# Optimization experiments

Hardware: AMD Instinct MI355X
Metric: run time of the kernel (lower is better)

The kernel has to match this reference:

```python
import jax, jax.numpy as jnp
import numpy as np
from jax.scipy.linalg import solve_triangular

B = 131072; OBS = 128; AD = 8; H = 64; FH = 32; NL = 4
D1 = AD // 2; D2 = AD - D1; TRIL = AD * (AD + 1) // 2
_rows, _cols = np.tril_indices(AD)          # same row-major order as torch.tril_indices
_diag = (_rows == _cols)                    # bool mask over TRIL entries
_diag_pos = np.where(_diag)[0]
LOG2PI = float(np.log(2.0 * np.pi))
EPS = float(np.finfo(np.float32).eps)       # torch RMSNorm default eps = finfo.eps


def _rms(x, w):
    return x * jax.lax.rsqrt(jnp.mean(x * x, axis=-1, keepdims=True) + EPS) * w


def setup_inputs() -> dict:
    ks = iter(jax.random.split(jax.random.key(0), 32))
    def w(shape, scale):
        return jax.random.normal(next(ks), shape, jnp.float32) * scale
    z = lambda *s: jnp.zeros(s, jnp.float32)
    return dict(
        x=jax.random.normal(next(ks), (B, OBS), jnp.float32),
        action=jax.random.normal(next(ks), (B, AD), jnp.float32),
        z_rpo=jax.random.uniform(next(ks), (B, AD), jnp.float32, -0.1, 0.1),
        cW1=w((OBS, H), OBS ** -0.5), cb1=z(H), c_rms=jnp.ones(H, jnp.float32),
        cW2=w((H, H), H ** -0.5), cb2=z(H), cW3=w((H, 1), H ** -0.5), cb3=z(1),
        aW1=w((OBS, H), OBS ** -0.5), ab1=z(H), aW2=w((H, H), H ** -0.5), ab2=z(H),
        mW=w((H, AD), 0.01), mb=z(AD),
        tW1=w((OBS, H), OBS ** -0.5), tb1=z(H), t_rms1=jnp.ones(H, jnp.float32),
        tW2=w((H, H), H ** -0.5), tb2=z(H), t_rms2=jnp.ones(H, jnp.float32),
        hW=w((H, TRIL), 0.01), hb=z(TRIL),
        fW1=w((NL, D1 + OBS, FH), (D1 + OBS) ** -0.5), fb1=z(NL, FH),
        fW2=w((NL, FH, 2 * D2), 0.01), fb2=z(NL, 2 * D2),
    )


def reference(x, action, z_rpo, cW1, cb1, c_rms, cW2, cb2, cW3, cb3,
              aW1, ab1, aW2, ab2, mW, mb,
              tW1, tb1, t_rms1, tW2, tb2, t_rms2, hW, hb,
              fW1, fb1, fW2, fb2):
    silu = jax.nn.silu
    Bn = x.shape[0]
    # actor mean trunk + head, with RPO uniform perturbation (action is given)
    h = silu(silu(x @ aW1 + ab1) @ aW2 + ab2)
    action_mean = h @ mW + mb + z_rpo
    # state-dependent lower-triangular covariance factor
    tl = _rms(silu(x @ tW1 + tb1), t_rms1)
    tl = _rms(silu(tl @ tW2 + tb2), t_rms2)
    raw = tl @ hW + hb                                   # [B, TRIL]
    proc = jnp.where(_diag, jax.nn.softplus(raw), raw)
    L = jnp.zeros((Bn, AD, AD), raw.dtype).at[:, _rows, _cols].set(proc)
    log_det_L = jnp.log(proc[:, _diag_pos]).sum(-1)      # [B]
    # coupling flow inverse: noise -> correlated
    noise = action - action_mean
    x1, x2 = noise[:, :D1], noise[:, D1:]
    fld = jnp.zeros((Bn,), raw.dtype)
    for i in reversed(range(NL)):
        cond, y = (x1, x2) if i % 2 == 0 else (x2, x1)
        st = silu(jnp.concatenate([cond, x], -1) @ fW1[i] + fb1[i]) @ fW2[i] + fb2[i]
        s_raw, tshift = jnp.split(st, 2, -1)
        s = jnp.tanh(s_raw) * 2.0
        xt = (y - tshift) * jnp.exp(-s)
        if i % 2 == 0:
            x2 = xt
        else:
            x1 = xt
        fld = fld + s.sum(-1)
    correlated = jnp.concatenate([x1, x2], -1)           # [B, AD]
    zc = solve_triangular(L, correlated[..., None], lower=True)[..., 0]
    mahal = (zc * zc).sum(-1)
    log_prob = -0.5 * (AD * LOG2PI + mahal) - log_det_L - fld
    entropy = 0.5 * (AD * (1.0 + LOG2PI)) + log_det_L + fld
    # critic
    v = _rms(silu(x @ cW1 + cb1), c_rms)
    v = silu(v @ cW2 + cb2) @ cW3 + cb3                  # [B, 1]
    return (action, log_prob, entropy, v)
```

## Files before the change

kernel.cpp:

```cpp
#include <hip/hip_runtime.h>
#include <hip/hip_bf16.h>

typedef __attribute__((ext_vector_type(8))) short    v8s;
typedef __attribute__((ext_vector_type(4))) float    f4;
typedef __attribute__((ext_vector_type(2))) float    f2;
typedef __attribute__((ext_vector_type(2))) unsigned u32x2;

#define MFMA16 __builtin_amdgcn_mfma_f32_16x16x32_bf16

#define AW1T 0
#define TW1T 8192
#define CW1T 16384
#define AW2T 24576
#define TW2T 28672
#define CW2T 32768
#define MWT  36864
#define HWT  37888
#define FW1XT 40960
#define FW2T  57344
#define WS_BF16_TOTAL 59392
#define W1CTO 0
#define HBPO  512

#define LOG2PI 1.83787706640934548356f
#define EPSF   1.1920928955078125e-07f

__device__ __constant__ int PERM[36] = {0,2,5,9,14,20,27,35,
  1,3,4,6,7,8,10,11,12,13,15,16,17,18,19,21,22,23,24,25,26,28,29,30,31,32,33,34};

__device__ __forceinline__ float ubits(unsigned u){union{unsigned u;float f;}c;c.u=u;return c.f;}
__device__ __forceinline__ unsigned fbits(float f){union{float f;unsigned u;}c;c.f=f;return c.u;}
__device__ __forceinline__ float rcpf(float x){ return __builtin_amdgcn_rcpf(x); }
__device__ __forceinline__ float siluf(float v){ return v * rcpf(1.f + __expf(-v)); }
__device__ __forceinline__ unsigned pk2(float a,float b){
  union{__hip_bfloat162 h; unsigned u;} cv;
  cv.h = __float22bfloat162_rn(make_float2(a,b));
  return cv.u;
}
__device__ __forceinline__ unsigned short f2bu(float a){
  unsigned ua=fbits(a); ua+=0x7fffu+((ua>>16)&1u);
  return (unsigned short)(ua>>16);
}
__device__ __forceinline__ float b2f16(unsigned short h){ return ubits(((unsigned)h)<<16); }
__device__ __forceinline__ float qsum(float v){
  v += __shfl_xor(v,16,64); v += __shfl_xor(v,32,64); return v;
}
__device__ __forceinline__ int swz(int row, int blk){ return row*64 + ((blk ^ (row&7))*8); }
__device__ __forceinline__ int swzx(int row, int blk){ return row*128 + ((blk ^ (row&7))*8); }
__device__ __forceinline__ int a2idx(int i, int n, int c){
  return ((((i<<5)+n)<<4) ^ ((n&8)<<1)) + (c ^ ((n&7)<<1));
}

__global__ __launch_bounds__(256)
void prep_kernel(const float* __restrict__ aW1, const float* __restrict__ aW2,
                 const float* __restrict__ mW,  const float* __restrict__ tW1,
                 const float* __restrict__ tW2, const float* __restrict__ hW,
                 const float* __restrict__ hb,  const float* __restrict__ cW1,
                 const float* __restrict__ cW2, const float* __restrict__ fW1,
                 const float* __restrict__ fW2,
                 unsigned short* __restrict__ ws16, float* __restrict__ wsf)
{
  const int tid = blockIdx.x*256 + threadIdx.x;
  const int stride = gridDim.x*256;
  for (int idx=tid; idx<64*128; idx+=stride){
    int f=idx>>9, r=idx&511, lane=r>>3, j=idx&7;
    int wt=f>>2, kt=f&3, c=lane&15, q=lane>>4;
    int n=wt*16+c, k=kt*32+q*8+j;
    ws16[AW1T+idx]=f2bu(aW1[k*64+n]);
    ws16[TW1T+idx]=f2bu(tW1[k*64+n]);
    ws16[CW1T+idx]=f2bu(cW1[k*64+n]);
  }
  for (int idx=tid; idx<64*64; idx+=stride){
    int f=idx>>9, r=idx&511, lane=r>>3, j=idx&7;
    int wt=f>>1, kt=f&1, c=lane&15, q=lane>>4;
    int n=wt*16+c, k=kt*32+q*8+j;
    ws16[AW2T+idx]=f2bu(aW2[k*64+n]);
    ws16[TW2T+idx]=f2bu(tW2[k*64+n]);
    ws16[CW2T+idx]=f2bu(cW2[k*64+n]);
  }
  for (int idx=tid; idx<16*64; idx+=stride){
    int f=idx>>9, r=idx&511, lane=r>>3, j=idx&7;
    int kt=f, c=lane&15, q=lane>>4;
    int n=c, k=kt*32+q*8+j;
    ws16[MWT+idx]=f2bu(n<8 ? mW[k*8+n] : 0.f);
  }
  for (int idx=tid; idx<48*64; idx+=stride){
    int f=idx>>9, r=idx&511, lane=r>>3, j=idx&7;
    int wt=f>>1, kt=f&1, c=lane&15, q=lane>>4;
    int n=wt*16+c, k=kt*32+q*8+j;
    ws16[HWT+idx]=f2bu(n<36 ? hW[k*36+PERM[n]] : 0.f);
  }
  for (int idx=tid; idx<4*32*128; idx+=stride){
    int i=idx>>12, rem=idx&4095;
    int f=rem>>9, r=rem&511, lane=r>>3, j=idx&7;
    int wt=f>>2, kt=f&3, c=lane&15, q=lane>>4;
    int n=wt*16+c, k=kt*32+q*8+j;
    ws16[FW1XT+idx]=f2bu(fW1[i*4224 + (4+k)*32 + n]);
  }
  for (int idx=tid; idx<4*16*32; idx+=stride){
    int i=idx>>9, r=idx&511, lane=r>>3, j=idx&7;
    int c=lane&15, q=lane>>4;
    int k=q*8+j;
    ws16[FW2T+idx]=f2bu(c<8 ? fW2[i*256 + k*8 + c] : 0.f);
  }
  for (int idx=tid; idx<4*32*4; idx+=stride){
    int i=idx>>7, rem=idx&127, n=rem>>2, k=rem&3;
    wsf[W1CTO+idx]=fW1[i*4224 + k*32 + n];
  }
  for (int idx=tid; idx<48; idx+=stride)
    wsf[HBPO+idx] = idx<36 ? hb[PERM[idx]] : 0.f;
}

template<int NWT>
__device__ __forceinline__ void gemmX(const unsigned short* __restrict__ Wt,
                                      const v8s* __restrict__ xf,
                                      f4 (*acc)[2], int lane)
{
#pragma unroll
  for (int kt=0; kt<4; ++kt){
    v8s wf[NWT];
#pragma unroll
    for (int wt=0; wt<NWT; ++wt)
      wf[wt] = *(const v8s*)(Wt + ((wt*4 + kt)*64 + lane)*8);
#pragma unroll
    for (int wt=0; wt<NWT; ++wt)
#pragma unroll
      for (int et=0; et<2; ++et)
        acc[wt][et] = MFMA16(wf[wt], xf[et*4+kt], acc[wt][et], 0,0,0);
  }
}

template<int NWT>
__device__ __forceinline__ void gemmH(const unsigned short* __restrict__ Wt,
                                      const unsigned short* __restrict__ actL,
                                      f4 (*acc)[2], int lane, int c, int q)
{
#pragma unroll
  for (int kt=0; kt<2; ++kt){
    v8s wf[NWT];
#pragma unroll
    for (int wt=0; wt<NWT; ++wt)
      wf[wt] = *(const v8s*)(Wt + ((wt*2 + kt)*64 + lane)*8);
    v8s af[2];
#pragma unroll
    for (int et=0; et<2; ++et)
      af[et] = *(const v8s*)(actL + swz(et*16+c, kt*4+q));
#pragma unroll
    for (int wt=0; wt<NWT; ++wt)
#pragma unroll
      for (int et=0; et<2; ++et)
        acc[wt][et] = MFMA16(wf[wt], af[et], acc[wt][et], 0,0,0);
  }
}

__global__ __launch_bounds__(128) __attribute__((amdgpu_waves_per_eu(3, 4)))
void policy_kernel(
    const float* __restrict__ x,    const float* __restrict__ action, const float* __restrict__ z_rpo,
    const float* __restrict__ cb1,  const float* __restrict__ c_rms,  const float* __restrict__ cb2,
    const float* __restrict__ cW3,  const float* __restrict__ cb3,
    const float* __restrict__ ab1,  const float* __restrict__ ab2,    const float* __restrict__ mb,
    const float* __restrict__ tb1,  const float* __restrict__ t_rms1, const float* __restrict__ tb2,
    const float* __restrict__ t_rms2,
    const float* __restrict__ fb1,  const float* __restrict__ fb2,
    const unsigned short* __restrict__ ws16, const float* __restrict__ wsf,
    float* __restrict__ out, const int Btot)
{
  const int tid  = threadIdx.x;
  const int wv   = tid >> 6;
  const int lane = tid & 63;
  const int q = lane >> 4, c = lane & 15;
  const int b0 = blockIdx.x << 5;

  __shared__ alignas(16) unsigned char smem[20352];
  unsigned*       a2b  = (unsigned*)smem;
  unsigned short* xL   = (unsigned short*)smem;
  unsigned short* act0 = (unsigned short*)(smem + 8192);
  unsigned short* act1 = (unsigned short*)(smem + 12288);
  unsigned short* triL = (unsigned short*)(smem + 16384);
  float*          nstL = (float*)(smem + 18688);
  unsigned short* amL  = (unsigned short*)(smem + 19712);
  float*          fldL = (float*)(smem + 20224);

  {
    const float* xb = x + (size_t)b0*128;
    const int rr = lane>>3, bb = (lane&7)*2;
#pragma unroll
    for (int rg=0; rg<2; ++rg){
      const int row = wv*16 + rg*8 + rr;
      const float* p = xb + row*128 + (lane&7)*16;
      f4 u0=*(const f4*)p, u1=*(const f4*)(p+4), u2=*(const f4*)(p+8), u3=*(const f4*)(p+12);
      union { unsigned u[4]; v8s v; } r0, r1;
      r0.u[0]=pk2(u0[0],u0[1]); r0.u[1]=pk2(u0[2],u0[3]);
      r0.u[2]=pk2(u1[0],u1[1]); r0.u[3]=pk2(u1[2],u1[3]);
      r1.u[0]=pk2(u2[0],u2[1]); r1.u[1]=pk2(u2[2],u2[3]);
      r1.u[2]=pk2(u3[0],u3[1]); r1.u[3]=pk2(u3[2],u3[3]);
      *(v8s*)(xL + swzx(row, bb  )) = r0.v;
      *(v8s*)(xL + swzx(row, bb+1)) = r1.v;
    }
  }
  const int l = lane;
  f4 a0v, a1v, zr0v, zr1v;
  if (wv==0 && l<32){
    const size_t bb = (size_t)(b0+l)*8;
    a0v=*(const f4*)(action+bb); a1v=*(const f4*)(action+bb+4);
    zr0v=*(const f4*)(z_rpo+bb); zr1v=*(const f4*)(z_rpo+bb+4);
    *(f4*)(out+bb)=a0v; *(f4*)(out+bb+4)=a1v;
  }
  __syncthreads();
  v8s xf[8];
#pragma unroll
  for (int et=0; et<2; ++et)
#pragma unroll
    for (int kt=0; kt<4; ++kt)
      xf[et*4+kt] = *(const v8s*)(xL + swzx(et*16+c, kt*4+q));
  __syncthreads();

  f4 acc[4][2];
  const f4 z4 = {0.f,0.f,0.f,0.f};
  float ldet[2], vv[2];
  float tri[36];

  if (wv == 0){
#pragma unroll
    for (int wt=0; wt<4; ++wt) for (int et=0; et<2; ++et) acc[wt][et]=z4;
    gemmX<4>(ws16+AW1T, xf, acc, lane);
#pragma unroll
    for (int wt=0; wt<4; ++wt){
      const f4 bv = *(const f4*)(ab1 + wt*16 + q*4);
#pragma unroll
      for (int et=0; et<2; ++et){
        float s0=siluf(acc[wt][et][0]+bv[0]), s1=siluf(acc[wt][et][1]+bv[1]);
        float s2=siluf(acc[wt][et][2]+bv[2]), s3=siluf(acc[wt][et][3]+bv[3]);
        u32x2 u = {pk2(s0,s1), pk2(s2,s3)};
        *(u32x2*)(act0 + swz(et*16+c, wt*2+(q>>1)) + (q&1)*4) = u;
      }
    }
#pragma unroll
    for (int wt=0; wt<4; ++wt) for (int et=0; et<2; ++et) acc[wt][et]=z4;
    gemmH<4>(ws16+AW2T, act0, acc, lane, c, q);
#pragma unroll
    for (int wt=0; wt<4; ++wt){
      const f4 bv = *(const f4*)(ab2 + wt*16 + q*4);
#pragma unroll
      for (int et=0; et<2; ++et){
        float s0=siluf(acc[wt][et][0]+bv[0]), s1=siluf(acc[wt][et][1]+bv[1]);
        float s2=siluf(acc[wt][et][2]+bv[2]), s3=siluf(acc[wt][et][3]+bv[3]);
        u32x2 u = {pk2(s0,s1), pk2(s2,s3)};
        *(u32x2*)(act0 + swz(et*16+c, wt*2+(q>>1)) + (q&1)*4) = u;
      }
    }
    {
      f4 am1[1][2]; am1[0][0]=z4; am1[0][1]=z4;
      gemmH<1>(ws16+MWT, act0, am1, lane, c, q);
      if (q<2){
        const f4 mbv = *(const f4*)(mb + q*4);
#pragma unroll
        for (int et=0; et<2; ++et){
          u32x2 u = {pk2(am1[0][et][0]+mbv[0], am1[0][et][1]+mbv[1]),
                     pk2(am1[0][et][2]+mbv[2], am1[0][et][3]+mbv[3])};
          *(u32x2*)(amL + (et*16+c)*8 + q*4) = u;
        }
      }
    }
  } else {
#pragma unroll
    for (int i=0; i<4; ++i){
      f4 a2[2][2];
#pragma unroll
      for (int wt=0; wt<2; ++wt) for (int et=0; et<2; ++et) a2[wt][et]=z4;
      gemmX<2>(ws16+FW1XT+i*4096, xf, a2, lane);
#pragma unroll
      for (int wt=0; wt<2; ++wt)
#pragma unroll
        for (int r=0; r<4; ++r){
          const int n = wt*16 + q*4 + r;
          a2b[a2idx(i, n, c)] = pk2(a2[wt][0][r], a2[wt][1][r]);
        }
    }
  }

  if (wv==0 && l<32){
    float nst[8];
#pragma unroll
    for (int j=0;j<4;++j){
      nst[j]   = a0v[j]-b2f16(amL[l*8+j])  -zr0v[j];
      nst[4+j] = a1v[j]-b2f16(amL[l*8+4+j])-zr1v[j];
    }
    *(f4*)(nstL + l*8)     = (f4){nst[0],nst[1],nst[2],nst[3]};
    *(f4*)(nstL + l*8 + 4) = (f4){nst[4],nst[5],nst[6],nst[7]};
  }

  __syncthreads();

  if (wv == 0){
    float fld = 0.f;
    const int e = l & 31, h = l >> 5, j0 = h*2;
#pragma unroll
    for (int ii=0; ii<4; ++ii){
      const int i = 3-ii;
      const int cb = (i&1)?4:0, yb = (i&1)?0:4;
      float nv[2][4];
#pragma unroll
      for (int et=0; et<2; ++et){
        const float* np = nstL + (et*16+c)*8 + cb;
        f2 t0=*(const f2*)np, t1=*(const f2*)(np+2);
        nv[et][0]=t0[0]; nv[et][1]=t0[1]; nv[et][2]=t1[0]; nv[et][3]=t1[1];
      }
#pragma unroll
      for (int wt=0; wt<2; ++wt){
        const f4 bv = *(const f4*)(fb1 + i*32 + wt*16 + q*4);
        float sh[2][4];
#pragma unroll
        for (int r=0; r<4; ++r){
          const int n = wt*16 + q*4 + r;
          const f4 wc = *(const f4*)(wsf + W1CTO + i*128 + n*4);
          const unsigned ua = a2b[a2idx(i, n, c)];
          const float a2e0 = b2f16((unsigned short)(ua & 0xffffu));
          const float a2e1 = b2f16((unsigned short)(ua >> 16));
          {
            float hv0 = a2e0 + bv[r]
                      + wc[0]*nv[0][0] + wc[1]*nv[0][1]
                      + wc[2]*nv[0][2] + wc[3]*nv[0][3];
            sh[0][r] = siluf(hv0);
            float hv1 = a2e1 + bv[r]
                      + wc[0]*nv[1][0] + wc[1]*nv[1][1]
                      + wc[2]*nv[1][2] + wc[3]*nv[1][3];
            sh[1][r] = siluf(hv1);
          }
        }
#pragma unroll
        for (int et=0; et<2; ++et){
          u32x2 u = {pk2(sh[et][0],sh[et][1]), pk2(sh[et][2],sh[et][3])};
          *(u32x2*)(act0 + swz(et*16+c, wt*2+(q>>1)) + (q&1)*4) = u;
        }
      }
      {
        const v8s wf3 = *(const v8s*)(ws16 + FW2T + i*512 + lane*8);
        f4 as[2];
#pragma unroll
        for (int et=0; et<2; ++et){
          const v8s hf = *(const v8s*)(act0 + swz(et*16+c, q));
          f4 a1s = z4;
          a1s = MFMA16(wf3, hf, a1s, 0,0,0);
          as[et]=a1s;
        }
        if (q<2){
          const f4 fbv = *(const f4*)(fb2 + i*8 + q*4);
#pragma unroll
          for (int et=0; et<2; ++et){
            u32x2 u = {pk2(as[et][0]+fbv[0], as[et][1]+fbv[1]),
                       pk2(as[et][2]+fbv[2], as[et][3]+fbv[3])};
            *(u32x2*)(amL + (et*16+c)*8 + q*4) = u;
          }
        }
      }
      {
        float sr0=b2f16(amL[e*8+j0  ]), sr1=b2f16(amL[e*8+j0+1]);
        float th0=b2f16(amL[e*8+4+j0]), th1=b2f16(amL[e*8+5+j0]);
        float s0=2.f-4.f*rcpf(__expf(2.f*sr0)+1.f);
        float s1=2.f-4.f*rcpf(__expf(2.f*sr1)+1.f);
        float n0=(nstL[e*8+yb+j0  ]-th0)*__expf(-s0);
        float n1=(nstL[e*8+yb+j0+1]-th1)*__expf(-s1);
        *(f2*)(nstL + e*8 + yb + j0) = (f2){n0,n1};
        fld += s0+s1;
      }
    }
    fld += __shfl_xor(fld, 32, 64);
    if (l < 32) fldL[l] = fld;
  } else {
#pragma unroll
    for (int wt=0; wt<4; ++wt) for (int et=0; et<2; ++et) acc[wt][et]=z4;
    gemmX<4>(ws16+TW1T, xf, acc, lane);
    float r1[2];
    {
      float ss[2]={0.f,0.f};
#pragma unroll
      for (int wt=0; wt<4; ++wt){
        const f4 bv = *(const f4*)(tb1 + wt*16 + q*4);
        const f4 rw = *(const f4*)(t_rms1 + wt*16 + q*4);
#pragma unroll
        for (int et=0; et<2; ++et){
          float s0=siluf(acc[wt][et][0]+bv[0]), s1=siluf(acc[wt][et][1]+bv[1]);
          float s2=siluf(acc[wt][et][2]+bv[2]), s3=siluf(acc[wt][et][3]+bv[3]);
          ss[et] += s0*s0+s1*s1+s2*s2+s3*s3;
          u32x2 u = {pk2(s0*rw[0],s1*rw[1]), pk2(s2*rw[2],s3*rw[3])};
          *(u32x2*)(act1 + swz(et*16+c, wt*2+(q>>1)) + (q&1)*4) = u;
        }
      }
#pragma unroll
      for (int et=0; et<2; ++et) r1[et]=rsqrtf(qsum(ss[et])*(1.f/64.f)+EPSF);
    }
#pragma unroll
    for (int wt=0; wt<4; ++wt) for (int et=0; et<2; ++et) acc[wt][et]=z4;
    gemmH<4>(ws16+TW2T, act1, acc, lane, c, q);
    float r2[2];
    {
      float ss[2]={0.f,0.f};
#pragma unroll
      for (int wt=0; wt<4; ++wt){
        const f4 bv = *(const f4*)(tb2 + wt*16 + q*4);
        const f4 rw = *(const f4*)(t_rms2 + wt*16 + q*4);
#pragma unroll
        for (int et=0; et<2; ++et){
          float s0=siluf(r1[et]*acc[wt][et][0]+bv[0]), s1=siluf(r1[et]*acc[wt][et][1]+bv[1]);
          float s2=siluf(r1[et]*acc[wt][et][2]+bv[2]), s3=siluf(r1[et]*acc[wt][et][3]+bv[3]);
          ss[et] += s0*s0+s1*s1+s2*s2+s3*s3;
          u32x2 u = {pk2(s0*rw[0],s1*rw[1]), pk2(s2*rw[2],s3*rw[3])};
          *(u32x2*)(act1 + swz(et*16+c, wt*2+(q>>1)) + (q&1)*4) = u;
        }
      }
#pragma unroll
      for (int et=0; et<2; ++et) r2[et]=rsqrtf(qsum(ss[et])*(1.f/64.f)+EPSF);
    }
    {
      f4 a3[3][2];
#pragma unroll
      for (int wt=0; wt<3; ++wt) for (int et=0; et<2; ++et) a3[wt][et]=z4;
      gemmH<3>(ws16+HWT, act1, a3, lane, c, q);
      float ldp[2]={0.f,0.f};
#pragma unroll
      for (int wt=0; wt<3; ++wt){
        const f4 hbv = *(const f4*)(wsf + HBPO + wt*16 + q*4);
#pragma unroll
        for (int et=0; et<2; ++et){
          float t0=r2[et]*a3[wt][et][0]+hbv[0], t1=r2[et]*a3[wt][et][1]+hbv[1];
          float t2=r2[et]*a3[wt][et][2]+hbv[2], t3=r2[et]*a3[wt][et][3]+hbv[3];
          if (wt==0 && q<2){
            t0=fmaxf(t0,0.f)+__logf(1.f+__expf(-fabsf(t0)));
            t1=fmaxf(t1,0.f)+__logf(1.f+__expf(-fabsf(t1)));
            t2=fmaxf(t2,0.f)+__logf(1.f+__expf(-fabsf(t2)));
            t3=fmaxf(t3,0.f)+__logf(1.f+__expf(-fabsf(t3)));
            ldp[et] += __logf(t0)+__logf(t1)+__logf(t2)+__logf(t3);
          }
          if (wt<2 || q==0){
            u32x2 u = {pk2(t0,t1), pk2(t2,t3)};
            *(u32x2*)(triL + (et*16+c)*36 + wt*16 + q*4) = u;
          }
        }
      }
#pragma unroll
      for (int et=0; et<2; ++et) ldet[et]=qsum(ldp[et]);
    }
#pragma unroll
    for (int wt=0; wt<4; ++wt) for (int et=0; et<2; ++et) acc[wt][et]=z4;
    gemmX<4>(ws16+CW1T, xf, acc, lane);
    float rc[2];
    {
      float ss[2]={0.f,0.f};
#pragma unroll
      for (int wt=0; wt<4; ++wt){
        const f4 bv = *(const f4*)(cb1 + wt*16 + q*4);
        const f4 rw = *(const f4*)(c_rms + wt*16 + q*4);
#pragma unroll
        for (int et=0; et<2; ++et){
          float s0=siluf(acc[wt][et][0]+bv[0]), s1=siluf(acc[wt][et][1]+bv[1]);
          float s2=siluf(acc[wt][et][2]+bv[2]), s3=siluf(acc[wt][et][3]+bv[3]);
          ss[et] += s0*s0+s1*s1+s2*s2+s3*s3;
          u32x2 u = {pk2(s0*rw[0],s1*rw[1]), pk2(s2*rw[2],s3*rw[3])};
          *(u32x2*)(act1 + swz(et*16+c, wt*2+(q>>1)) + (q&1)*4) = u;
        }
      }
#pragma unroll
      for (int et=0; et<2; ++et) rc[et]=rsqrtf(qsum(ss[et])*(1.f/64.f)+EPSF);
    }
    {
#pragma unroll
      for (int wt=0; wt<4; ++wt) for (int et=0; et<2; ++et) acc[wt][et]=z4;
      gemmH<4>(ws16+CW2T, act1, acc, lane, c, q);
      float vp[2]={0.f,0.f};
#pragma unroll
      for (int wt=0; wt<4; ++wt){
        const f4 bv = *(const f4*)(cb2 + wt*16 + q*4);
        const f4 wvv = *(const f4*)(cW3 + wt*16 + q*4);
#pragma unroll
        for (int et=0; et<2; ++et){
          vp[et] = fmaf(siluf(rc[et]*acc[wt][et][0]+bv[0]), wvv[0], vp[et]);
          vp[et] = fmaf(siluf(rc[et]*acc[wt][et][1]+bv[1]), wvv[1], vp[et]);
          vp[et] = fmaf(siluf(rc[et]*acc[wt][et][2]+bv[2]), wvv[2], vp[et]);
          vp[et] = fmaf(siluf(rc[et]*acc[wt][et][3]+bv[3]), wvv[3], vp[et]);
        }
      }
      const float cb3v = cb3[0];
#pragma unroll
      for (int et=0; et<2; ++et) vv[et]=qsum(vp[et])+cb3v;
    }
    if (l < 32){
      constexpr int INVPERM[36] = {0,8,1,9,10,2,11,12,13,3,14,15,16,17,4,18,19,20,
                                   21,22,5,23,24,25,26,27,28,6,29,30,31,32,33,34,35,7};
#pragma unroll
      for (int j=0;j<36;++j) tri[j] = b2f16(triL[l*36 + INVPERM[j]]);
    }
  }

  __syncthreads();

  if (wv==1 && l<32){
    float nf[8];
#pragma unroll
    for (int j=0;j<8;++j) nf[j] = nstL[l*8+j];
    const float fldv = fldL[l];
    float zv[8], mahal=0.f;
#pragma unroll
    for (int r=0;r<8;++r){
      float s=nf[r];
      const int base=(r*(r+1))>>1;
#pragma unroll
      for (int cc=0;cc<r;++cc) s -= tri[base+cc]*zv[cc];
      const float z = s*rcpf(tri[base+r]);
      zv[r]=z; mahal+=z*z;
    }
    const float ldet_s = (l<16)?ldet[0]:ldet[1];
    const float v_s    = (l<16)?vv[0]:vv[1];
    const float lp = -0.5f*(8.f*LOG2PI+mahal) - ldet_s - fldv;
    const float en =  0.5f*(8.f*(1.f+LOG2PI)) + ldet_s + fldv;
    out[(size_t)Btot*8  + b0 + l] = lp;
    out[(size_t)Btot*9  + b0 + l] = en;
    out[(size_t)Btot*10 + b0 + l] = v_s;
  }
}

extern "C" void kernel_launch(void* const* d_in, const int* in_sizes, int n_in,
                              void* d_out, int out_size, void* d_ws, size_t ws_size,
                              hipStream_t stream) {
  const float* x      = (const float*)d_in[0];
  const float* action = (const float*)d_in[1];
  const float* z_rpo  = (const float*)d_in[2];
  const float* cW1    = (const float*)d_in[3];
  const float* cb1    = (const float*)d_in[4];
  const float* c_rms  = (const float*)d_in[5];
  const float* cW2    = (const float*)d_in[6];
  const float* cb2    = (const float*)d_in[7];
  const float* cW3    = (const float*)d_in[8];
  const float* cb3    = (const float*)d_in[9];
  const float* aW1    = (const float*)d_in[10];
  const float* ab1    = (const float*)d_in[11];
  const float* aW2    = (const float*)d_in[12];
  const float* ab2    = (const float*)d_in[13];
  const float* mW     = (const float*)d_in[14];
  const float* mb     = (const float*)d_in[15];
  const float* tW1    = (const float*)d_in[16];
  const float* tb1    = (const float*)d_in[17];
  const float* t_rms1 = (const float*)d_in[18];
  const float* tW2    = (const float*)d_in[19];
  const float* tb2    = (const float*)d_in[20];
  const float* t_rms2 = (const float*)d_in[21];
  const float* hW     = (const float*)d_in[22];
  const float* hb     = (const float*)d_in[23];
  const float* fW1    = (const float*)d_in[24];
  const float* fb1    = (const float*)d_in[25];
  const float* fW2    = (const float*)d_in[26];
  const float* fb2    = (const float*)d_in[27];
  float* out = (float*)d_out;

  unsigned short* ws16 = (unsigned short*)d_ws;
  float* wsf = (float*)((char*)d_ws + WS_BF16_TOTAL*2);

  const int Btot = in_sizes[0] / 128;

  hipLaunchKernelGGL(prep_kernel, dim3(128), dim3(256), 0, stream,
                     aW1, aW2, mW, tW1, tW2, hW, hb, cW1, cW2, fW1, fW2, ws16, wsf);
  hipLaunchKernelGGL(policy_kernel, dim3(Btot/32), dim3(128), 0, stream,
                     x, action, z_rpo, cb1, c_rms, cb2, cW3, cb3,
                     ab1, ab2, mb, tb1, t_rms1, tb2, t_rms2, fb1, fb2,
                     ws16, wsf, out, Btot);
}
```

Before: 190.5 us.

## Split per-block work across four waves and parallelize flow coupling over two waves

The block grows from 2 to 4 waves. Each MLP trunk (actor, flow W1 precompute, tril, critic) now gets its own wave instead of being serialized on two waves. The coupling-flow inverse is split across two waves, each handling 16 samples, and the triangular solve moves to the tril wave with the value passed through shared memory. This shortens the serial critical path per block, at the cost of more LDS per block and an extra barrier, plus possible occupancy changes from the larger block.

Result: slower. 203.0 us (+6.6%).

```diff
diff --git a/kernel.cpp b/kernel.cpp
--- a/kernel.cpp
+++ b/kernel.cpp
@@ -153,7 +153,7 @@
   }
 }
 
-__global__ __launch_bounds__(128) __attribute__((amdgpu_waves_per_eu(3, 4)))
+__global__ __launch_bounds__(256) __attribute__((amdgpu_waves_per_eu(3, 8)))
 void policy_kernel(
     const float* __restrict__ x,    const float* __restrict__ action, const float* __restrict__ z_rpo,
     const float* __restrict__ cb1,  const float* __restrict__ c_rms,  const float* __restrict__ cb2,
@@ -171,32 +171,31 @@
   const int q = lane >> 4, c = lane & 15;
   const int b0 = blockIdx.x << 5;
 
-  __shared__ alignas(16) unsigned char smem[20352];
+  __shared__ alignas(16) unsigned char smem[24576];
   unsigned*       a2b  = (unsigned*)smem;
   unsigned short* xL   = (unsigned short*)smem;
   unsigned short* act0 = (unsigned short*)(smem + 8192);
   unsigned short* act1 = (unsigned short*)(smem + 12288);
-  unsigned short* triL = (unsigned short*)(smem + 16384);
-  float*          nstL = (float*)(smem + 18688);
-  unsigned short* amL  = (unsigned short*)(smem + 19712);
-  float*          fldL = (float*)(smem + 20224);
+  unsigned short* act2 = (unsigned short*)(smem + 16384);
+  unsigned short* triL = (unsigned short*)(smem + 20480);
+  float*          nstL = (float*)(smem + 22784);
+  unsigned short* amL  = (unsigned short*)(smem + 23808);
+  float*          fldL = (float*)(smem + 24320);
+  float*          vvL  = (float*)(smem + 24448);
 
   {
     const float* xb = x + (size_t)b0*128;
     const int rr = lane>>3, bb = (lane&7)*2;
-#pragma unroll
-    for (int rg=0; rg<2; ++rg){
-      const int row = wv*16 + rg*8 + rr;
-      const float* p = xb + row*128 + (lane&7)*16;
-      f4 u0=*(const f4*)p, u1=*(const f4*)(p+4), u2=*(const f4*)(p+8), u3=*(const f4*)(p+12);
-      union { unsigned u[4]; v8s v; } r0, r1;
-      r0.u[0]=pk2(u0[0],u0[1]); r0.u[1]=pk2(u0[2],u0[3]);
-      r0.u[2]=pk2(u1[0],u1[1]); r0.u[3]=pk2(u1[2],u1[3]);
-      r1.u[0]=pk2(u2[0],u2[1]); r1.u[1]=pk2(u2[2],u2[3]);
-      r1.u[2]=pk2(u3[0],u3[1]); r1.u[3]=pk2(u3[2],u3[3]);
-      *(v8s*)(xL + swzx(row, bb  )) = r0.v;
-      *(v8s*)(xL + swzx(row, bb+1)) = r1.v;
-    }
+    const int row = wv*8 + rr;
+    const float* p = xb + row*128 + (lane&7)*16;
+    f4 u0=*(const f4*)p, u1=*(const f4*)(p+4), u2=*(const f4*)(p+8), u3=*(const f4*)(p+12);
+    union { unsigned u[4]; v8s v; } r0, r1;
+    r0.u[0]=pk2(u0[0],u0[1]); r0.u[1]=pk2(u0[2],u0[3]);
+    r0.u[2]=pk2(u1[0],u1[1]); r0.u[3]=pk2(u1[2],u1[3]);
+    r1.u[0]=pk2(u2[0],u2[1]); r1.u[1]=pk2(u2[2],u2[3]);
+    r1.u[2]=pk2(u3[0],u3[1]); r1.u[3]=pk2(u3[2],u3[3]);
+    *(v8s*)(xL + swzx(row, bb  )) = r0.v;
+    *(v8s*)(xL + swzx(row, bb+1)) = r1.v;
   }
   const int l = lane;
   f4 a0v, a1v, zr0v, zr1v;
@@ -215,12 +214,11 @@
       xf[et*4+kt] = *(const v8s*)(xL + swzx(et*16+c, kt*4+q));
   __syncthreads();
 
-  f4 acc[4][2];
   const f4 z4 = {0.f,0.f,0.f,0.f};
-  float ldet[2], vv[2];
-  float tri[36];
+  float ldet[2];
 
   if (wv == 0){
+    f4 acc[4][2];
 #pragma unroll
     for (int wt=0; wt<4; ++wt) for (int et=0; et<2; ++et) acc[wt][et]=z4;
     gemmX<4>(ws16+AW1T, xf, acc, lane);
@@ -262,7 +260,17 @@
         }
       }
     }
-  } else {
+    if (l<32){
+      float nst[8];
+#pragma unroll
+      for (int j=0;j<4;++j){
+        nst[j]   = a0v[j]-b2f16(amL[l*8+j])  -zr0v[j];
+        nst[4+j] = a1v[j]-b2f16(amL[l*8+4+j])-zr1v[j];
+      }
+      *(f4*)(nstL + l*8)     = (f4){nst[0],nst[1],nst[2],nst[3]};
+      *(f4*)(nstL + l*8 + 4) = (f4){nst[4],nst[5],nst[6],nst[7]};
+    }
+  } else if (wv == 1){
 #pragma unroll
     for (int i=0; i<4; ++i){
       f4 a2[2][2];
@@ -277,97 +285,8 @@
           a2b[a2idx(i, n, c)] = pk2(a2[wt][0][r], a2[wt][1][r]);
         }
     }
-  }
-
-  if (wv==0 && l<32){
-    float nst[8];
-#pragma unroll
-    for (int j=0;j<4;++j){
-      nst[j]   = a0v[j]-b2f16(amL[l*8+j])  -zr0v[j];
-      nst[4+j] = a1v[j]-b2f16(amL[l*8+4+j])-zr1v[j];
-    }
-    *(f4*)(nstL + l*8)     = (f4){nst[0],nst[1],nst[2],nst[3]};
-    *(f4*)(nstL + l*8 + 4) = (f4){nst[4],nst[5],nst[6],nst[7]};
-  }
-
-  __syncthreads();
-
-  if (wv == 0){
-    float fld = 0.f;
-    const int e = l & 31, h = l >> 5, j0 = h*2;
-#pragma unroll
-    for (int ii=0; ii<4; ++ii){
-      const int i = 3-ii;
-      const int cb = (i&1)?4:0, yb = (i&1)?0:4;
-      float nv[2][4];
-#pragma unroll
-      for (int et=0; et<2; ++et){
-        const float* np = nstL + (et*16+c)*8 + cb;
-        f2 t0=*(const f2*)np, t1=*(const f2*)(np+2);
-        nv[et][0]=t0[0]; nv[et][1]=t0[1]; nv[et][2]=t1[0]; nv[et][3]=t1[1];
-      }
-#pragma unroll
-      for (int wt=0; wt<2; ++wt){
-        const f4 bv = *(const f4*)(fb1 + i*32 + wt*16 + q*4);
-        float sh[2][4];
-#pragma unroll
-        for (int r=0; r<4; ++r){
-          const int n = wt*16 + q*4 + r;
-          const f4 wc = *(const f4*)(wsf + W1CTO + i*128 + n*4);
-          const unsigned ua = a2b[a2idx(i, n, c)];
-          const float a2e0 = b2f16((unsigned short)(ua & 0xffffu));
-          const float a2e1 = b2f16((unsigned short)(ua >> 16));
-          {
-            float hv0 = a2e0 + bv[r]
-                      + wc[0]*nv[0][0] + wc[1]*nv[0][1]
-                      + wc[2]*nv[0][2] + wc[3]*nv[0][3];
-            sh[0][r] = siluf(hv0);
-            float hv1 = a2e1 + bv[r]
-                      + wc[0]*nv[1][0] + wc[1]*nv[1][1]
-                      + wc[2]*nv[1][2] + wc[3]*nv[1][3];
-            sh[1][r] = siluf(hv1);
-          }
-        }
-#pragma unroll
-        for (int et=0; et<2; ++et){
-          u32x2 u = {pk2(sh[et][0],sh[et][1]), pk2(sh[et][2],sh[et][3])};
-          *(u32x2*)(act0 + swz(et*16+c, wt*2+(q>>1)) + (q&1)*4) = u;
-        }
-      }
-      {
-        const v8s wf3 = *(const v8s*)(ws16 + FW2T + i*512 + lane*8);
-        f4 as[2];
-#pragma unroll
-        for (int et=0; et<2; ++et){
-          const v8s hf = *(const v8s*)(act0 + swz(et*16+c, q));
-          f4 a1s = z4;
-          a1s = MFMA16(wf3, hf, a1s, 0,0,0);
-          as[et]=a1s;
-        }
-        if (q<2){
-          const f4 fbv = *(const f4*)(fb2 + i*8 + q*4);
-#pragma unroll
-          for (int et=0; et<2; ++et){
-            u32x2 u = {pk2(as[et][0]+fbv[0], as[et][1]+fbv[1]),
-                       pk2(as[et][2]+fbv[2], as[et][3]+fbv[3])};
-            *(u32x2*)(amL + (et*16+c)*8 + q*4) = u;
-          }
-        }
-      }
-      {
-        float sr0=b2f16(amL[e*8+j0  ]), sr1=b2f16(amL[e*8+j0+1]);
-        float th0=b2f16(amL[e*8+4+j0]), th1=b2f16(amL[e*8+5+j0]);
-        float s0=2.f-4.f*rcpf(__expf(2.f*sr0)+1.f);
-        float s1=2.f-4.f*rcpf(__expf(2.f*sr1)+1.f);
-        float n0=(nstL[e*8+yb+j0  ]-th0)*__expf(-s0);
-        float n1=(nstL[e*8+yb+j0+1]-th1)*__expf(-s1);
-        *(f2*)(nstL + e*8 + yb + j0) = (f2){n0,n1};
-        fld += s0+s1;
-      }
-    }
-    fld += __shfl_xor(fld, 32, 64);
-    if (l < 32) fldL[l] = fld;
-  } else {
+  } else if (wv == 2){
+    f4 acc[4][2];
 #pragma unroll
     for (int wt=0; wt<4; ++wt) for (int et=0; et<2; ++et) acc[wt][et]=z4;
     gemmX<4>(ws16+TW1T, xf, acc, lane);
@@ -441,6 +360,8 @@
 #pragma unroll
       for (int et=0; et<2; ++et) ldet[et]=qsum(ldp[et]);
     }
+  } else {
+    f4 acc[4][2];
 #pragma unroll
     for (int wt=0; wt<4; ++wt) for (int et=0; et<2; ++et) acc[wt][et]=z4;
     gemmX<4>(ws16+CW1T, xf, acc, lane);
@@ -457,16 +378,17 @@
           float s2=siluf(acc[wt][et][2]+bv[2]), s3=siluf(acc[wt][et][3]+bv[3]);
           ss[et] += s0*s0+s1*s1+s2*s2+s3*s3;
           u32x2 u = {pk2(s0*rw[0],s1*rw[1]), pk2(s2*rw[2],s3*rw[3])};
-          *(u32x2*)(act1 + swz(et*16+c, wt*2+(q>>1)) + (q&1)*4) = u;
+          *(u32x2*)(act2 + swz(et*16+c, wt*2+(q>>1)) + (q&1)*4) = u;
         }
       }
 #pragma unroll
       for (int et=0; et<2; ++et) rc[et]=rsqrtf(qsum(ss[et])*(1.f/64.f)+EPSF);
     }
     {
-#pragma unroll
-      for (int wt=0; wt<4; ++wt) for (int et=0; et<2; ++et) acc[wt][et]=z4;
-      gemmH<4>(ws16+CW2T, act1, acc, lane, c, q);
+      f4 acc2[4][2];
+#pragma unroll
+      for (int wt=0; wt<4; ++wt) for (int et=0; et<2; ++et) acc2[wt][et]=z4;
+      gemmH<4>(ws16+CW2T, act2, acc2, lane, c, q);
       float vp[2]={0.f,0.f};
 #pragma unroll
       for (int wt=0; wt<4; ++wt){
@@ -474,27 +396,82 @@
         const f4 wvv = *(const f4*)(cW3 + wt*16 + q*4);
 #pragma unroll
         for (int et=0; et<2; ++et){
-          vp[et] = fmaf(siluf(rc[et]*acc[wt][et][0]+bv[0]), wvv[0], vp[et]);
-          vp[et] = fmaf(siluf(rc[et]*acc[wt][et][1]+bv[1]), wvv[1], vp[et]);
-          vp[et] = fmaf(siluf(rc[et]*acc[wt][et][2]+bv[2]), wvv[2], vp[et]);
-          vp[et] = fmaf(siluf(rc[et]*acc[wt][et][3]+bv[3]), wvv[3], vp[et]);
+          vp[et] = fmaf(siluf(rc[et]*acc2[wt][et][0]+bv[0]), wvv[0], vp[et]);
+          vp[et] = fmaf(siluf(rc[et]*acc2[wt][et][1]+bv[1]), wvv[1], vp[et]);
+          vp[et] = fmaf(siluf(rc[et]*acc2[wt][et][2]+bv[2]), wvv[2], vp[et]);
+          vp[et] = fmaf(siluf(rc[et]*acc2[wt][et][3]+bv[3]), wvv[3], vp[et]);
         }
       }
       const float cb3v = cb3[0];
-#pragma unroll
-      for (int et=0; et<2; ++et) vv[et]=qsum(vp[et])+cb3v;
-    }
-    if (l < 32){
-      constexpr int INVPERM[36] = {0,8,1,9,10,2,11,12,13,3,14,15,16,17,4,18,19,20,
-                                   21,22,5,23,24,25,26,27,28,6,29,30,31,32,33,34,35,7};
-#pragma unroll
-      for (int j=0;j<36;++j) tri[j] = b2f16(triL[l*36 + INVPERM[j]]);
+      const float v0 = qsum(vp[0]);
+      const float v1 = qsum(vp[1]);
+      if (l<16){ vvL[l]=v0+cb3v; vvL[16+l]=v1+cb3v; }
     }
   }
 
   __syncthreads();
 
-  if (wv==1 && l<32){
+  if (wv < 2){
+    const int e  = wv*16 + c;
+    const int eu = wv*16 + (l&15);
+    const int ju = l>>4;
+    float fld = 0.f;
+#pragma unroll
+    for (int ii=0; ii<4; ++ii){
+      const int i = 3-ii;
+      const int cb = (i&1)?4:0, yb = (i&1)?0:4;
+      f2 t0=*(const f2*)(nstL + e*8 + cb), t1=*(const f2*)(nstL + e*8 + cb + 2);
+      const float nv0=t0[0], nv1=t0[1], nv2=t1[0], nv3=t1[1];
+#pragma unroll
+      for (int wt=0; wt<2; ++wt){
+        const f4 bv = *(const f4*)(fb1 + i*32 + wt*16 + q*4);
+        float sh[4];
+#pragma unroll
+        for (int r=0; r<4; ++r){
+          const int n = wt*16 + q*4 + r;
+          const f4 wc = *(const f4*)(wsf + W1CTO + i*128 + n*4);
+          const unsigned ua = a2b[a2idx(i, n, c)];
+          const float a2e = b2f16(wv==0 ? (unsigned short)(ua & 0xffffu)
+                                        : (unsigned short)(ua >> 16));
+          float hv = a2e + bv[r] + wc[0]*nv0 + wc[1]*nv1 + wc[2]*nv2 + wc[3]*nv3;
+          sh[r] = siluf(hv);
+        }
+        u32x2 u = {pk2(sh[0],sh[1]), pk2(sh[2],sh[3])};
+        *(u32x2*)(act0 + swz(e, wt*2+(q>>1)) + (q&1)*4) = u;
+      }
+      {
+        const v8s wf3 = *(const v8s*)(ws16 + FW2T + i*512 + lane*8);
+        const v8s hf = *(const v8s*)(act0 + swz(e, q));
+        f4 a1s = z4;
+        a1s = MFMA16(wf3, hf, a1s, 0,0,0);
+        if (q<2){
+          const f4 fbv = *(const f4*)(fb2 + i*8 + q*4);
+          u32x2 u = {pk2(a1s[0]+fbv[0], a1s[1]+fbv[1]),
+                     pk2(a1s[2]+fbv[2], a1s[3]+fbv[3])};
+          *(u32x2*)(amL + e*8 + q*4) = u;
+        }
+      }
+      {
+        float sr = b2f16(amL[eu*8+ju]);
+        float th = b2f16(amL[eu*8+4+ju]);
+        float s  = 2.f-4.f*rcpf(__expf(2.f*sr)+1.f);
+        float n  = (nstL[eu*8+yb+ju]-th)*__expf(-s);
+        nstL[eu*8+yb+ju] = n;
+        fld += s;
+      }
+    }
+    fld = qsum(fld);
+    if (l < 16) fldL[wv*16 + l] = fld;
+  }
+
+  __syncthreads();
+
+  if (wv==2 && l<32){
+    constexpr int INVPERM[36] = {0,8,1,9,10,2,11,12,13,3,14,15,16,17,4,18,19,20,
+                                 21,22,5,23,24,25,26,27,28,6,29,30,31,32,33,34,35,7};
+    float tri[36];
+#pragma unroll
+    for (int j=0;j<36;++j) tri[j] = b2f16(triL[l*36 + INVPERM[j]]);
     float nf[8];
 #pragma unroll
     for (int j=0;j<8;++j) nf[j] = nstL[l*8+j];
@@ -510,7 +487,7 @@
       zv[r]=z; mahal+=z*z;
     }
     const float ldet_s = (l<16)?ldet[0]:ldet[1];
-    const float v_s    = (l<16)?vv[0]:vv[1];
+    const float v_s    = vvL[l];
     const float lp = -0.5f*(8.f*LOG2PI+mahal) - ldet_s - fldv;
     const float en =  0.5f*(8.f*(1.f+LOG2PI)) + ldet_s + fldv;
     out[(size_t)Btot*8  + b0 + l] = lp;
@@ -559,7 +536,7 @@
 
   hipLaunchKernelGGL(prep_kernel, dim3(128), dim3(256), 0, stream,
                      aW1, aW2, mW, tW1, tW2, hW, hb, cW1, cW2, fW1, fW2, ws16, wsf);
-  hipLaunchKernelGGL(policy_kernel, dim3(Btot/32), dim3(128), 0, stream,
+  hipLaunchKernelGGL(policy_kernel, dim3(Btot/32), dim3(256), 0, stream,
                      x, action, z_rpo, cb1, c_rms, cb2, cW3, cb3,
                      ab1, ab2, mb, tb1, t_rms1, tb2, t_rms2, fb1, fb2,
                      ws16, wsf, out, Btot);
```
